# Kernel optimization log

Measured on AMD Instinct MI355X. Metric: run time of the kernel, lower is better.

The kernel has to match this reference:

```python
import jax, jax.numpy as jnp
import numpy as np

D_MODEL = 1024
NHEAD = 16
HEAD_DIM = D_MODEL // NHEAD  # 64
AXIS_DIM = HEAD_DIM // 4     # 16
DFF = 4096
EPS = 1e-5
BASE = 10000.0
B, S = 4, 2048


def setup_inputs() -> dict:
    key = jax.random.key(0)
    ks = jax.random.split(key, 10)
    def xavier(k, shape):
        fan_in, fan_out = shape[1], shape[0]
        limit = np.sqrt(6.0 / (fan_in + fan_out))
        return jax.random.uniform(k, shape, jnp.float32, -limit, limit)
    return {
        "src": jax.random.normal(ks[0], (B, S, D_MODEL), jnp.float32),
        "positions": jax.random.normal(ks[1], (B, S, 4), jnp.float32),
        "w_qkv": xavier(ks[2], (3 * D_MODEL, D_MODEL)),
        "w_out": xavier(ks[3], (D_MODEL, D_MODEL)),
        "norm1_w": jnp.ones((D_MODEL,), jnp.float32),
        "norm2_w": jnp.ones((D_MODEL,), jnp.float32),
        "w1": xavier(ks[4], (DFF, D_MODEL)),
        "w2": xavier(ks[5], (D_MODEL, DFF)),
        "w3": xavier(ks[6], (DFF, D_MODEL)),
        "axis_scale": jnp.ones((4,), jnp.float32),
    }


def _rmsnorm(x, w, eps=EPS):
    return x * jax.lax.rsqrt(jnp.mean(x * x, axis=-1, keepdims=True) + eps) * w


def _rope_rotate(x, cos, sin):
    # x: (B,H,S,HEAD_DIM); cos/sin: (B,1,S,4,AXIS_DIM//2)
    b, h, s, _ = x.shape
    xr = x.reshape(b, h, s, 4, AXIS_DIM // 2, 2)  # 4 axis chunks, interleaved pairs
    e, o = xr[..., 0], xr[..., 1]
    re = e * cos - o * sin
    ro = o * cos + e * sin
    return jnp.stack([re, ro], axis=-1).reshape(b, h, s, HEAD_DIM)


def reference(src, positions, w_qkv, w_out, norm1_w, norm2_w, w1, w2, w3, axis_scale):
    b, s, _ = src.shape
    x = src
    x_norm = _rmsnorm(x, norm1_w)
    qkv = x_norm @ w_qkv.T  # (B,S,3*D)
    qkv = qkv.reshape(b, s, 3, NHEAD, HEAD_DIM).transpose(2, 0, 3, 1, 4)
    q, k, v = qkv[0], qkv[1], qkv[2]  # (B,H,S,Dh)

    # 4D RoPE: same inv_freq per axis (base^{-idx/axis_dim})
    inv_freq = BASE ** (-(jnp.arange(0, AXIS_DIM, 2, dtype=jnp.float32) / AXIS_DIM))  # (8,)
    coord = positions * axis_scale  # (B,S,4)
    angles = coord[..., None] * inv_freq  # (B,S,4,8)
    cos = jnp.cos(angles)[:, None]  # (B,1,S,4,8)
    sin = jnp.sin(angles)[:, None]
    q = _rope_rotate(q, cos, sin)
    k = _rope_rotate(k, cos, sin)

    scale = 1.0 / jnp.sqrt(jnp.float32(HEAD_DIM))
    scores = jnp.einsum("bhqd,bhkd->bhqk", q, k) * scale
    attn = jax.nn.softmax(scores, axis=-1)
    attn_out = jnp.einsum("bhqk,bhkd->bhqd", attn, v)
    attn_out = attn_out.transpose(0, 2, 1, 3).reshape(b, s, D_MODEL)
    x = x + attn_out @ w_out.T

    x_norm = _rmsnorm(x, norm2_w)
    ff = (jax.nn.silu(x_norm @ w1.T) * (x_norm @ w3.T)) @ w2.T
    return x + ff
```

## Files before the change

### kernel.cpp

```cpp
#include <hip/hip_runtime.h>

typedef unsigned short u16;
typedef __attribute__((ext_vector_type(4))) unsigned short u16x4;
typedef __attribute__((ext_vector_type(8))) short bf16x8;
typedef __attribute__((ext_vector_type(4))) float f32x4;
typedef __attribute__((ext_vector_type(16))) float f32x16;

__device__ __forceinline__ float bf2f(u16 u) {
  union { unsigned i; float f; } v; v.i = ((unsigned)u) << 16; return v.f;
}
__device__ __forceinline__ u16 f2bf(float f) {
  union { float f; unsigned i; } v; v.f = f;
  unsigned r = v.i + 0x7fffu + ((v.i >> 16) & 1u);
  return (u16)(r >> 16);
}
__device__ __forceinline__ void gl_lds16(const u16* g, u16* l) {
  __builtin_amdgcn_global_load_lds((const __attribute__((address_space(1))) unsigned*)g,
                                   (__attribute__((address_space(3))) unsigned*)l, 16, 0, 0);
}
__device__ __forceinline__ f32x16 mfma32(bf16x8 a, bf16x8 b, f32x16 c) {
  return __builtin_amdgcn_mfma_f32_32x32x16_bf16(a, b, c, 0, 0, 0);
}

__global__ __launch_bounds__(256) void k_cvt(const float* __restrict__ S,
                                             u16* __restrict__ D, int n) {
  int i = (blockIdx.x * 256 + threadIdx.x) * 8;
  if (i >= n) return;
  f32x4 a = *(const f32x4*)(S + i), b = *(const f32x4*)(S + i + 4);
  bf16x8 r;
  r[0] = (short)f2bf(a.x); r[1] = (short)f2bf(a.y); r[2] = (short)f2bf(a.z); r[3] = (short)f2bf(a.w);
  r[4] = (short)f2bf(b.x); r[5] = (short)f2bf(b.y); r[6] = (short)f2bf(b.z); r[7] = (short)f2bf(b.w);
  *(bf16x8*)(D + i) = r;
}

__global__ __launch_bounds__(256) void k_rmsnorm(const void* __restrict__ X,
                                                 const float* __restrict__ W,
                                                 u16* __restrict__ Y, int x_ext) {
  const int tok = blockIdx.x, t = threadIdx.x;
  float x0, x1, x2, x3;
  if (x_ext) {
    f32x4 xv = ((const f32x4*)X)[tok * 256 + t];
    x0 = xv.x; x1 = xv.y; x2 = xv.z; x3 = xv.w;
  } else {
    u16x4 xv = ((const u16x4*)X)[tok * 256 + t];
    x0 = bf2f(xv.x); x1 = bf2f(xv.y); x2 = bf2f(xv.z); x3 = bf2f(xv.w);
  }
  float ss = x0 * x0 + x1 * x1 + x2 * x2 + x3 * x3;
#pragma unroll
  for (int m = 32; m; m >>= 1) ss += __shfl_xor(ss, m);
  __shared__ float red[4];
  if ((t & 63) == 0) red[t >> 6] = ss;
  __syncthreads();
  float inv = rsqrtf((red[0] + red[1] + red[2] + red[3]) * (1.f / 1024.f) + 1e-5f);
  f32x4 wv = ((const f32x4*)W)[t];
  u16x4 o;
  o.x = f2bf(x0 * inv * wv.x);
  o.y = f2bf(x1 * inv * wv.y);
  o.z = f2bf(x2 * inv * wv.z);
  o.w = f2bf(x3 * inv * wv.w);
  ((u16x4*)(Y + (size_t)tok * 1024))[t] = o;
}

template <int EPI, int OUTF32>
__global__ __launch_bounds__(256, 2) void k_gemm(const u16* __restrict__ A,
                                                 const u16* __restrict__ W,
                                                 const void* R, void* C,
                                                 int M, int N, int K, int r_ext) {
  __shared__ u16 sA[128 * 32];
  __shared__ u16 sB[128 * 32];
  const int t = threadIdx.x;
  const int wid = t >> 6, lane = t & 63, quad = lane >> 4, l16 = lane & 15;
  const int wm = wid >> 1, wn = wid & 1;
  const size_t m0 = (size_t)blockIdx.y * 128, n0 = (size_t)blockIdx.x * 128;
  f32x4 acc[4][4] = {};
  const int srow = t >> 2, schunk = t & 3;
  const u16* Ag = A + (m0 + srow) * K + schunk * 8;
  const u16* Wg = W + (n0 + srow) * (size_t)K + schunk * 8;
  u16* sAw = sA + wid * 512;
  u16* sBw = sB + wid * 512;
  for (int k0 = 0; k0 < K; k0 += 32) {
    gl_lds16(Ag + k0, sAw);
    gl_lds16(Ag + (size_t)64 * K + k0, sAw + 2048);
    gl_lds16(Wg + k0, sBw);
    gl_lds16(Wg + (size_t)64 * K + k0, sBw + 2048);
    __syncthreads();
    bf16x8 a[4], b[4];
#pragma unroll
    for (int mt = 0; mt < 4; ++mt)
      a[mt] = *(const bf16x8*)(sA + (wm * 64 + mt * 16 + l16) * 32 + quad * 8);
#pragma unroll
    for (int nt = 0; nt < 4; ++nt)
      b[nt] = *(const bf16x8*)(sB + (wn * 64 + nt * 16 + l16) * 32 + quad * 8);
#pragma unroll
    for (int mt = 0; mt < 4; ++mt)
#pragma unroll
      for (int nt = 0; nt < 4; ++nt)
        acc[mt][nt] = __builtin_amdgcn_mfma_f32_16x16x32_bf16(a[mt], b[nt], acc[mt][nt], 0, 0, 0);
    __syncthreads();
  }
#pragma unroll
  for (int mt = 0; mt < 4; ++mt) {
#pragma unroll
    for (int nt = 0; nt < 4; ++nt) {
      size_t row = m0 + wm * 64 + mt * 16 + quad * 4;
      size_t col = n0 + wn * 64 + nt * 16 + l16;
#pragma unroll
      for (int r = 0; r < 4; ++r) {
        float v = acc[mt][nt][r];
        size_t idx = (row + r) * N + col;
        if (EPI == 1) v += r_ext ? ((const float*)R)[idx] : bf2f(((const u16*)R)[idx]);
        if (EPI == 2) { float h = bf2f(((const u16*)R)[idx]); v *= h / (1.f + __expf(-h)); }
        if (OUTF32) ((float*)C)[idx] = v;
        else ((u16*)C)[idx] = f2bf(v);
      }
    }
  }
}

__global__ __launch_bounds__(256) void k_rope(const u16* __restrict__ QKV,
                                              const float* __restrict__ POS,
                                              const float* __restrict__ ASC,
                                              u16* __restrict__ Qr, u16* __restrict__ Kr,
                                              u16* __restrict__ Vt) {
  const int bh = blockIdx.x, b = bh >> 4, h = bh & 15;
  const int s0 = blockIdx.y * 128;
  const int t = threadIdx.x;
  const int pr = t & 31, a = pr >> 3, f = pr & 7, srow = t >> 5;
  const float asc = ASC[a];
  const float invf = exp2f(-(float)f * (13.28771237954945f / 8.f));
  for (int pass = 0; pass < 16; ++pass) {
    int s = s0 + pass * 8 + srow;
    float ang = POS[((size_t)b * 2048 + s) * 4 + a] * asc * invf;
    float sn, cs;
    sincosf(ang, &sn, &cs);
    size_t ib = ((size_t)b * 2048 + s) * 3072 + h * 64 + a * 16 + f * 2;
    size_t ob = ((size_t)bh * 2048 + s) * 64 + a * 16 + f * 2;
    unsigned qw = *(const unsigned*)(QKV + ib);
    float e = bf2f((u16)(qw & 0xffff)), o = bf2f((u16)(qw >> 16));
    *(unsigned*)(Qr + ob) = (unsigned)f2bf(e * cs - o * sn) | ((unsigned)f2bf(o * cs + e * sn) << 16);
    unsigned kw = *(const unsigned*)(QKV + ib + 1024);
    e = bf2f((u16)(kw & 0xffff));
    o = bf2f((u16)(kw >> 16));
    *(unsigned*)(Kr + ob) = (unsigned)f2bf(e * cs - o * sn) | ((unsigned)f2bf(o * cs + e * sn) << 16);
  }
  __shared__ u16 vt[64 * 130];
#pragma unroll
  for (int it = 0; it < 32; ++it) {
    int idx = it * 256 + t, sl = idx >> 6, d = idx & 63;
    vt[d * 130 + sl] = QKV[((size_t)b * 2048 + s0 + sl) * 3072 + 2048 + h * 64 + d];
  }
  __syncthreads();
#pragma unroll
  for (int it = 0; it < 32; ++it) {
    int idx = it * 256 + t, d = idx >> 7, sl = idx & 127;
    Vt[((size_t)bh * 64 + d) * 2048 + s0 + sl] = vt[d * 130 + sl];
  }
}

#define SCL 0.18033688011112042f

__global__ __launch_bounds__(256, 2) void k_attn(const u16* __restrict__ Qr,
                                                 const u16* __restrict__ Kr,
                                                 const u16* __restrict__ Vt,
                                                 u16* __restrict__ O) {
  __shared__ u16 sK[2][4096];
  __shared__ u16 sV[2][4096];
  const int t = threadIdx.x, wid = t >> 6, lane = t & 63;
  const int il = lane & 31, hh = lane >> 5;
  const int bh = blockIdx.x;
  const int q0 = blockIdx.y * 256 + wid * 64;
  const size_t base = (size_t)bh * 2048 * 64;

  bf16x8 qf[2][4];
#pragma unroll
  for (int qt = 0; qt < 2; ++qt)
#pragma unroll
    for (int c = 0; c < 4; ++c)
      qf[qt][c] = *(const bf16x8*)(Qr + base + (size_t)(q0 + qt * 32 + il) * 64 + c * 16 + hh * 8);

  const f32x16 ZERO = {};
  f32x16 oa[2][2] = {{ZERO, ZERO}, {ZERO, ZERO}};
  float m[2] = {-1e30f, -1e30f}, lr[2] = {0.f, 0.f};

  const u16* Kb = Kr + base;
  const u16* Vb = Vt + base;
  const int cc = t & 7, r0 = t >> 3;
  {
    bf16x8 k0 = *(const bf16x8*)(Kb + (size_t)r0 * 64 + cc * 8);
    bf16x8 k1 = *(const bf16x8*)(Kb + (size_t)(r0 + 32) * 64 + cc * 8);
    bf16x8 v0 = *(const bf16x8*)(Vb + (size_t)r0 * 2048 + cc * 8);
    bf16x8 v1 = *(const bf16x8*)(Vb + (size_t)(r0 + 32) * 2048 + cc * 8);
    *(bf16x8*)(sK[0] + (cc * 64 + (r0 ^ cc)) * 8) = k0;
    *(bf16x8*)(sK[0] + (cc * 64 + ((r0 + 32) ^ cc)) * 8) = k1;
    *(bf16x8*)(sV[0] + (cc * 64 + (r0 ^ cc)) * 8) = v0;
    *(bf16x8*)(sV[0] + (cc * 64 + ((r0 + 32) ^ cc)) * 8) = v1;
  }
  __syncthreads();

  for (int it = 0; it < 32; ++it) {
    const u16* kb = sK[it & 1];
    const u16* vb = sV[it & 1];
    bf16x8 nk0, nk1, nv0, nv1;
    const int last = (it == 31);
    if (!last) {
      int kv = (it + 1) * 64;
      nk0 = *(const bf16x8*)(Kb + (size_t)(kv + r0) * 64 + cc * 8);
      nk1 = *(const bf16x8*)(Kb + (size_t)(kv + r0 + 32) * 64 + cc * 8);
      nv0 = *(const bf16x8*)(Vb + (size_t)r0 * 2048 + kv + cc * 8);
      nv1 = *(const bf16x8*)(Vb + (size_t)(r0 + 32) * 2048 + kv + cc * 8);
    }
    f32x16 sacc[2][2];
    __builtin_amdgcn_s_setprio(1);
#pragma unroll
    for (int kt = 0; kt < 2; ++kt) {
#pragma unroll
      for (int c = 0; c < 4; ++c) {
        int ch = c * 2 + hh;
        bf16x8 kf = *(const bf16x8*)(kb + (ch * 64 + ((kt * 32 + il) ^ ch)) * 8);
        if (c == 0) {
          sacc[0][kt] = mfma32(kf, qf[0][0], ZERO);
          sacc[1][kt] = mfma32(kf, qf[1][0], ZERO);
        } else {
          sacc[0][kt] = mfma32(kf, qf[0][c], sacc[0][kt]);
          sacc[1][kt] = mfma32(kf, qf[1][c], sacc[1][kt]);
        }
      }
    }
    __builtin_amdgcn_s_setprio(0);
    bf16x8 pa[2][4];
#pragma unroll
    for (int qt = 0; qt < 2; ++qt) {
      float mx = -1e30f;
#pragma unroll
      for (int kt = 0; kt < 2; ++kt)
#pragma unroll
        for (int r = 0; r < 16; ++r) mx = fmaxf(mx, sacc[qt][kt][r]);
      mx = fmaxf(mx, __shfl_xor(mx, 32));
      if (!__all(mx - m[qt] <= 64.f)) {
        float mn = fmaxf(m[qt], mx);
        float corr = exp2f((m[qt] - mn) * SCL);
        m[qt] = mn;
        lr[qt] *= corr;
#pragma unroll
        for (int dt = 0; dt < 2; ++dt)
#pragma unroll
          for (int r = 0; r < 16; ++r) oa[qt][dt][r] *= corr;
      }
      float mm = m[qt];
#pragma unroll
      for (int kt = 0; kt < 2; ++kt) {
        float p[16];
        float ls = 0.f;
#pragma unroll
        for (int r = 0; r < 16; ++r) {
          p[r] = exp2f((sacc[qt][kt][r] - mm) * SCL);
          ls += p[r];
        }
        lr[qt] += ls;
        unsigned w[8];
#pragma unroll
        for (int i = 0; i < 8; ++i)
          asm("v_cvt_pk_bf16_f32 %0, %1, %2" : "=v"(w[i]) : "v"(p[2 * i]), "v"(p[2 * i + 1]));
        asm("v_permlane32_swap_b32 %0, %1" : "+v"(w[0]), "+v"(w[2]));
        asm("v_permlane32_swap_b32 %0, %1" : "+v"(w[1]), "+v"(w[3]));
        asm("v_permlane32_swap_b32 %0, %1" : "+v"(w[4]), "+v"(w[6]));
        asm("v_permlane32_swap_b32 %0, %1" : "+v"(w[5]), "+v"(w[7]));
        union { unsigned u[4]; bf16x8 v; } f0, f1;
        f0.u[0] = w[0]; f0.u[1] = w[1]; f0.u[2] = w[2]; f0.u[3] = w[3];
        f1.u[0] = w[4]; f1.u[1] = w[5]; f1.u[2] = w[6]; f1.u[3] = w[7];
        pa[qt][kt * 2] = f0.v;
        pa[qt][kt * 2 + 1] = f1.v;
      }
    }
    __builtin_amdgcn_s_setprio(1);
#pragma unroll
    for (int ks = 0; ks < 4; ++ks) {
      int sc = ks * 2 + hh;
#pragma unroll
      for (int dt = 0; dt < 2; ++dt) {
        bf16x8 vf = *(const bf16x8*)(vb + (sc * 64 + ((dt * 32 + il) ^ sc)) * 8);
        oa[0][dt] = mfma32(vf, pa[0][ks], oa[0][dt]);
        oa[1][dt] = mfma32(vf, pa[1][ks], oa[1][dt]);
      }
    }
    __builtin_amdgcn_s_setprio(0);
    if (!last) {
      u16* kn = sK[(it + 1) & 1];
      u16* vn = sV[(it + 1) & 1];
      *(bf16x8*)(kn + (cc * 64 + (r0 ^ cc)) * 8) = nk0;
      *(bf16x8*)(kn + (cc * 64 + ((r0 + 32) ^ cc)) * 8) = nk1;
      *(bf16x8*)(vn + (cc * 64 + (r0 ^ cc)) * 8) = nv0;
      *(bf16x8*)(vn + (cc * 64 + ((r0 + 32) ^ cc)) * 8) = nv1;
    }
    __syncthreads();
  }
  const int b = bh >> 4, hd = bh & 15;
#pragma unroll
  for (int qt = 0; qt < 2; ++qt) {
    float lt = lr[qt] + __shfl_xor(lr[qt], 32);
    float inv = 1.f / lt;
    int q = q0 + qt * 32 + il;
#pragma unroll
    for (int dt = 0; dt < 2; ++dt) {
#pragma unroll
      for (int g = 0; g < 4; ++g) {
        u16x4 pk;
        pk.x = f2bf(oa[qt][dt][4 * g + 0] * inv);
        pk.y = f2bf(oa[qt][dt][4 * g + 1] * inv);
        pk.z = f2bf(oa[qt][dt][4 * g + 2] * inv);
        pk.w = f2bf(oa[qt][dt][4 * g + 3] * inv);
        *(u16x4*)(O + ((size_t)b * 2048 + q) * 1024 + hd * 64 + dt * 32 + 8 * g + 4 * hh) = pk;
      }
    }
  }
}

extern "C" void kernel_launch(void* const* d_in, const int* in_sizes, int n_in,
                              void* d_out, int out_size, void* d_ws, size_t ws_size,
                              hipStream_t stream) {
  const float* src    = (const float*)d_in[0];
  const float* pos    = (const float*)d_in[1];
  const float* w_qkv  = (const float*)d_in[2];
  const float* w_out  = (const float*)d_in[3];
  const float* n1w    = (const float*)d_in[4];
  const float* n2w    = (const float*)d_in[5];
  const float* w1     = (const float*)d_in[6];
  const float* w2     = (const float*)d_in[7];
  const float* w3     = (const float*)d_in[8];
  const float* ascale = (const float*)d_in[9];
  char* ws = (char*)d_ws;
  u16* xn  = (u16*)(ws);
  u16* qkv = (u16*)(ws + ((size_t)16 << 20));
  u16* Qr  = (u16*)(ws);
  u16* Kr  = (u16*)(ws + ((size_t)64 << 20));
  u16* Vt  = (u16*)(ws + ((size_t)80 << 20));
  u16* att = (u16*)(ws + ((size_t)16 << 20));
  u16* x   = (u16*)(ws + ((size_t)80 << 20));
  u16* xn2 = (u16*)(ws);
  u16* h1  = (u16*)(ws + ((size_t)16 << 20));
  u16* bqkv = (u16*)(ws + ((size_t)96 << 20));
  u16* bout = (u16*)(ws + ((size_t)102 << 20));
  u16* b1   = (u16*)(ws + ((size_t)104 << 20));
  u16* b3   = (u16*)(ws + ((size_t)112 << 20));
  u16* b2   = (u16*)(ws + ((size_t)120 << 20));

  k_cvt<<<1536, 256, 0, stream>>>(w_qkv, bqkv, 3145728);
  k_cvt<<<512,  256, 0, stream>>>(w_out, bout, 1048576);
  k_cvt<<<2048, 256, 0, stream>>>(w1, b1, 4194304);
  k_cvt<<<2048, 256, 0, stream>>>(w3, b3, 4194304);
  k_cvt<<<2048, 256, 0, stream>>>(w2, b2, 4194304);

  k_rmsnorm<<<8192, 256, 0, stream>>>(src, n1w, xn, 1);
  k_gemm<0, 0><<<dim3(24, 64), 256, 0, stream>>>(xn, bqkv, nullptr, qkv, 8192, 3072, 1024, 0);
  k_rope<<<dim3(64, 16), 256, 0, stream>>>(qkv, pos, ascale, Qr, Kr, Vt);
  k_attn<<<dim3(64, 8), 256, 0, stream>>>(Qr, Kr, Vt, att);
  k_gemm<1, 0><<<dim3(8, 64), 256, 0, stream>>>(att, bout, src, x, 8192, 1024, 1024, 1);
  k_rmsnorm<<<8192, 256, 0, stream>>>(x, n2w, xn2, 0);
  k_gemm<0, 0><<<dim3(32, 64), 256, 0, stream>>>(xn2, b1, nullptr, h1, 8192, 4096, 1024, 0);
  k_gemm<2, 0><<<dim3(32, 64), 256, 0, stream>>>(xn2, b3, h1, h1, 8192, 4096, 1024, 0);
  k_gemm<1, 1><<<dim3(8, 64), 256, 0, stream>>>(h1, b2, x, d_out, 8192, 1024, 4096, 0);
}
```

Baseline: 740.1 us.

## Add 256x256-tile double-buffered GEMM kernel for QKV and FFN up projections

Introduces a new 512-thread GEMM with 256x256 output tiles, double-buffered LDS loads via global_load_lds, and split MFMA phases with setprio/barrier interleaving. It replaces the 128-tile GEMM for the QKV projection and the w1/w3 FFN projections. The larger tile raises arithmetic intensity and overlaps the next tile's loads with compute, at the cost of more registers per thread (acc[8][4]), more LDS, and fewer blocks in flight.

After: 794.6 us. 1.07x slower.

```diff
diff --git a/kernel.cpp b/kernel.cpp
--- a/kernel.cpp
+++ b/kernel.cpp
@@ -112,6 +112,90 @@
         if (EPI == 2) { float h = bf2f(((const u16*)R)[idx]); v *= h / (1.f + __expf(-h)); }
         if (OUTF32) ((float*)C)[idx] = v;
         else ((u16*)C)[idx] = f2bf(v);
+      }
+    }
+  }
+}
+
+template <int EPI>
+__global__ __launch_bounds__(512, 2) void k_gemm256(const u16* __restrict__ A,
+                                                    const u16* __restrict__ W,
+                                                    const void* R, void* C,
+                                                    int M, int N, int K) {
+  __shared__ u16 sA[2][8192];
+  __shared__ u16 sB[2][8192];
+  const int t = threadIdx.x, lane = t & 63, wid = t >> 6;
+  const int quad = lane >> 4, l16 = lane & 15;
+  const int wm = wid >> 2, wn = wid & 3;
+  const size_t m0 = (size_t)blockIdx.y * 256, n0 = (size_t)blockIdx.x * 256;
+  f32x4 acc[8][4] = {};
+  const u16* AgLo = A + (m0 + wid * 16 + l16) * (size_t)K + quad * 8;
+  const u16* AgHi = A + (m0 + (wid + 8) * 16 + l16) * (size_t)K + quad * 8;
+  const u16* WgLo = W + (n0 + wid * 16 + l16) * (size_t)K + quad * 8;
+  const u16* WgHi = W + (n0 + (wid + 8) * 16 + l16) * (size_t)K + quad * 8;
+  const int ntiles = K >> 5;
+  gl_lds16(AgLo, &sA[0][wid * 512]);
+  gl_lds16(AgHi, &sA[0][(wid + 8) * 512]);
+  gl_lds16(WgLo, &sB[0][wid * 512]);
+  gl_lds16(WgHi, &sB[0][(wid + 8) * 512]);
+  __syncthreads();
+  for (int kt = 0; kt < ntiles; ++kt) {
+    const int b = kt & 1, nb = b ^ 1;
+    const int kn = (kt + 1) << 5;
+    const u16* sAb = sA[b];
+    const u16* sBb = sB[b];
+    bf16x8 af[8], bf[4];
+#pragma unroll
+    for (int i = 0; i < 4; ++i)
+      af[i] = *(const bf16x8*)(sAb + (wm * 8 + i) * 512 + lane * 8);
+#pragma unroll
+    for (int j = 0; j < 4; ++j)
+      bf[j] = *(const bf16x8*)(sBb + (wn * 4 + j) * 512 + lane * 8);
+    if (kt + 1 < ntiles) {
+      gl_lds16(AgLo + kn, &sA[nb][wid * 512]);
+      gl_lds16(AgHi + kn, &sA[nb][(wid + 8) * 512]);
+      gl_lds16(WgLo + kn, &sB[nb][wid * 512]);
+      gl_lds16(WgHi + kn, &sB[nb][(wid + 8) * 512]);
+    }
+    __builtin_amdgcn_s_barrier();
+    asm volatile("s_waitcnt lgkmcnt(0)" ::: "memory");
+    __builtin_amdgcn_sched_barrier(0);
+    __builtin_amdgcn_s_setprio(1);
+#pragma unroll
+    for (int i = 0; i < 4; ++i)
+#pragma unroll
+      for (int j = 0; j < 4; ++j)
+        acc[i][j] = __builtin_amdgcn_mfma_f32_16x16x32_bf16(af[i], bf[j], acc[i][j], 0, 0, 0);
+    __builtin_amdgcn_s_setprio(0);
+    __builtin_amdgcn_s_barrier();
+#pragma unroll
+    for (int i = 0; i < 4; ++i)
+      af[4 + i] = *(const bf16x8*)(sAb + (wm * 8 + 4 + i) * 512 + lane * 8);
+    __builtin_amdgcn_s_barrier();
+    asm volatile("s_waitcnt lgkmcnt(0)" ::: "memory");
+    __builtin_amdgcn_sched_barrier(0);
+    __builtin_amdgcn_s_setprio(1);
+#pragma unroll
+    for (int i = 0; i < 4; ++i)
+#pragma unroll
+      for (int j = 0; j < 4; ++j)
+        acc[4 + i][j] = __builtin_amdgcn_mfma_f32_16x16x32_bf16(af[4 + i], bf[j], acc[4 + i][j], 0, 0, 0);
+    __builtin_amdgcn_s_setprio(0);
+    asm volatile("s_waitcnt vmcnt(0)" ::: "memory");
+    __builtin_amdgcn_s_barrier();
+  }
+#pragma unroll
+  for (int mt = 0; mt < 8; ++mt) {
+#pragma unroll
+    for (int nt = 0; nt < 4; ++nt) {
+      size_t row = m0 + wm * 128 + mt * 16 + quad * 4;
+      size_t col = n0 + wn * 64 + nt * 16 + l16;
+#pragma unroll
+      for (int r = 0; r < 4; ++r) {
+        float v = acc[mt][nt][r];
+        size_t idx = (row + r) * N + col;
+        if (EPI == 2) { float h = bf2f(((const u16*)R)[idx]); v *= h / (1.f + __expf(-h)); }
+        ((u16*)C)[idx] = f2bf(v);
       }
     }
   }
@@ -351,12 +435,12 @@
   k_cvt<<<2048, 256, 0, stream>>>(w2, b2, 4194304);
 
   k_rmsnorm<<<8192, 256, 0, stream>>>(src, n1w, xn, 1);
-  k_gemm<0, 0><<<dim3(24, 64), 256, 0, stream>>>(xn, bqkv, nullptr, qkv, 8192, 3072, 1024, 0);
+  k_gemm256<0><<<dim3(12, 32), 512, 0, stream>>>(xn, bqkv, nullptr, qkv, 8192, 3072, 1024);
   k_rope<<<dim3(64, 16), 256, 0, stream>>>(qkv, pos, ascale, Qr, Kr, Vt);
   k_attn<<<dim3(64, 8), 256, 0, stream>>>(Qr, Kr, Vt, att);
   k_gemm<1, 0><<<dim3(8, 64), 256, 0, stream>>>(att, bout, src, x, 8192, 1024, 1024, 1);
   k_rmsnorm<<<8192, 256, 0, stream>>>(x, n2w, xn2, 0);
-  k_gemm<0, 0><<<dim3(32, 64), 256, 0, stream>>>(xn2, b1, nullptr, h1, 8192, 4096, 1024, 0);
-  k_gemm<2, 0><<<dim3(32, 64), 256, 0, stream>>>(xn2, b3, h1, h1, 8192, 4096, 1024, 0);
+  k_gemm256<0><<<dim3(16, 32), 512, 0, stream>>>(xn2, b1, nullptr, h1, 8192, 4096, 1024);
+  k_gemm256<2><<<dim3(16, 32), 512, 0, stream>>>(xn2, b3, h1, h1, 8192, 4096, 1024);
   k_gemm<1, 1><<<dim3(8, 64), 256, 0, stream>>>(h1, b2, x, d_out, 8192, 1024, 4096, 0);
 }
```

## Fuse W1 and W3 FFN GEMMs with SiLU gating into one kernel

Applied to the files above, without the earlier changes.

Replaces the two separate FFN up-projection GEMMs (W1 then W3 with a SiLU-gate epilogue reading h1) with a single kernel that loads each A tile once and accumulates both products side by side. The gate is applied in registers before one bf16 store. This removes a second read of the activations, the intermediate h1 write and read-back, and one launch. In exchange it doubles the accumulator registers per thread (128 floats), which may limit occupancy or cause spills despite the launch bound of 2.

Measured after the change: 699.5 us. -5.5%, faster.

```diff
diff --git a/kernel.cpp b/kernel.cpp
--- a/kernel.cpp
+++ b/kernel.cpp
@@ -109,9 +109,72 @@
         float v = acc[mt][nt][r];
         size_t idx = (row + r) * N + col;
         if (EPI == 1) v += r_ext ? ((const float*)R)[idx] : bf2f(((const u16*)R)[idx]);
-        if (EPI == 2) { float h = bf2f(((const u16*)R)[idx]); v *= h / (1.f + __expf(-h)); }
         if (OUTF32) ((float*)C)[idx] = v;
         else ((u16*)C)[idx] = f2bf(v);
+      }
+    }
+  }
+}
+
+__global__ __launch_bounds__(256, 2) void k_ffn(const u16* __restrict__ A,
+                                                const u16* __restrict__ W1,
+                                                const u16* __restrict__ W3,
+                                                u16* __restrict__ C,
+                                                int M, int N, int K) {
+  __shared__ u16 sA[128 * 32];
+  __shared__ u16 sB1[128 * 32];
+  __shared__ u16 sB3[128 * 32];
+  const int t = threadIdx.x;
+  const int wid = t >> 6, lane = t & 63, quad = lane >> 4, l16 = lane & 15;
+  const int wm = wid >> 1, wn = wid & 1;
+  const size_t m0 = (size_t)blockIdx.y * 128, n0 = (size_t)blockIdx.x * 128;
+  f32x4 acc1[4][4] = {};
+  f32x4 acc3[4][4] = {};
+  const int srow = t >> 2, schunk = t & 3;
+  const u16* Ag = A + (m0 + srow) * K + schunk * 8;
+  const u16* W1g = W1 + (n0 + srow) * (size_t)K + schunk * 8;
+  const u16* W3g = W3 + (n0 + srow) * (size_t)K + schunk * 8;
+  u16* sAw = sA + wid * 512;
+  u16* sB1w = sB1 + wid * 512;
+  u16* sB3w = sB3 + wid * 512;
+  for (int k0 = 0; k0 < K; k0 += 32) {
+    gl_lds16(Ag + k0, sAw);
+    gl_lds16(Ag + (size_t)64 * K + k0, sAw + 2048);
+    gl_lds16(W1g + k0, sB1w);
+    gl_lds16(W1g + (size_t)64 * K + k0, sB1w + 2048);
+    gl_lds16(W3g + k0, sB3w);
+    gl_lds16(W3g + (size_t)64 * K + k0, sB3w + 2048);
+    __syncthreads();
+    bf16x8 a[4], b1[4], b3[4];
+#pragma unroll
+    for (int mt = 0; mt < 4; ++mt)
+      a[mt] = *(const bf16x8*)(sA + (wm * 64 + mt * 16 + l16) * 32 + quad * 8);
+#pragma unroll
+    for (int nt = 0; nt < 4; ++nt) {
+      b1[nt] = *(const bf16x8*)(sB1 + (wn * 64 + nt * 16 + l16) * 32 + quad * 8);
+      b3[nt] = *(const bf16x8*)(sB3 + (wn * 64 + nt * 16 + l16) * 32 + quad * 8);
+    }
+#pragma unroll
+    for (int mt = 0; mt < 4; ++mt)
+#pragma unroll
+      for (int nt = 0; nt < 4; ++nt) {
+        acc1[mt][nt] = __builtin_amdgcn_mfma_f32_16x16x32_bf16(a[mt], b1[nt], acc1[mt][nt], 0, 0, 0);
+        acc3[mt][nt] = __builtin_amdgcn_mfma_f32_16x16x32_bf16(a[mt], b3[nt], acc3[mt][nt], 0, 0, 0);
+      }
+    __syncthreads();
+  }
+#pragma unroll
+  for (int mt = 0; mt < 4; ++mt) {
+#pragma unroll
+    for (int nt = 0; nt < 4; ++nt) {
+      size_t row = m0 + wm * 64 + mt * 16 + quad * 4;
+      size_t col = n0 + wn * 64 + nt * 16 + l16;
+#pragma unroll
+      for (int r = 0; r < 4; ++r) {
+        float v1 = acc1[mt][nt][r];
+        float v3 = acc3[mt][nt][r];
+        float h = v1 / (1.f + __expf(-v1)) * v3;
+        C[(row + r) * N + col] = f2bf(h);
       }
     }
   }
@@ -356,7 +419,6 @@
   k_attn<<<dim3(64, 8), 256, 0, stream>>>(Qr, Kr, Vt, att);
   k_gemm<1, 0><<<dim3(8, 64), 256, 0, stream>>>(att, bout, src, x, 8192, 1024, 1024, 1);
   k_rmsnorm<<<8192, 256, 0, stream>>>(x, n2w, xn2, 0);
-  k_gemm<0, 0><<<dim3(32, 64), 256, 0, stream>>>(xn2, b1, nullptr, h1, 8192, 4096, 1024, 0);
-  k_gemm<2, 0><<<dim3(32, 64), 256, 0, stream>>>(xn2, b3, h1, h1, 8192, 4096, 1024, 0);
+  k_ffn<<<dim3(32, 64), 256, 0, stream>>>(xn2, b1, b3, h1, 8192, 4096, 1024);
   k_gemm<1, 1><<<dim3(8, 64), 256, 0, stream>>>(h1, b2, x, d_out, 8192, 1024, 4096, 0);
 }
```
